# Optimization experiments

Hardware: AMD Instinct MI355X
Metric: run time of the kernel (lower is better)

The kernel has to match this reference:

```python
import jax, jax.numpy as jnp
import numpy as np

B, T, D_IN = 1024, 512, 32   # batch, sequence_length, input_dim
H = 512                      # hidden_dim
P = 96                       # prediction_length
D_OUT = 1                    # output_dim


def setup_inputs() -> dict:
    key = jax.random.key(0)
    ks = jax.random.split(key, 24)
    s = 1.0 / np.sqrt(H)  # PyTorch GRU default init scale
    u = lambda k, shape: jax.random.uniform(k, shape, jnp.float32, -s, s)
    inp = {"x": jax.random.normal(ks[0], (B, T, D_IN), jnp.float32)}
    # Encoder GRU: layer0 input D_IN, layer1 input H. Gate order: r, z, n.
    inp["enc_Wih0"] = u(ks[1], (3 * H, D_IN)); inp["enc_Whh0"] = u(ks[2], (3 * H, H))
    inp["enc_bih0"] = u(ks[3], (3 * H,));      inp["enc_bhh0"] = u(ks[4], (3 * H,))
    inp["enc_Wih1"] = u(ks[5], (3 * H, H));    inp["enc_Whh1"] = u(ks[6], (3 * H, H))
    inp["enc_bih1"] = u(ks[7], (3 * H,));      inp["enc_bhh1"] = u(ks[8], (3 * H,))
    # Decoder GRU: layer0 input D_OUT, layer1 input H.
    inp["dec_Wih0"] = u(ks[9], (3 * H, D_OUT)); inp["dec_Whh0"] = u(ks[10], (3 * H, H))
    inp["dec_bih0"] = u(ks[11], (3 * H,));      inp["dec_bhh0"] = u(ks[12], (3 * H,))
    inp["dec_Wih1"] = u(ks[13], (3 * H, H));    inp["dec_Whh1"] = u(ks[14], (3 * H, H))
    inp["dec_bih1"] = u(ks[15], (3 * H,));      inp["dec_bhh1"] = u(ks[16], (3 * H,))
    # Output projection + learned decoder start token.
    inp["out_W"] = u(ks[17], (D_OUT, H)); inp["out_b"] = u(ks[18], (D_OUT,))
    inp["dec_start"] = jnp.zeros((1, 1, D_OUT), jnp.float32)
    return inp


def gru_cell(x, h, Wih, Whh, bih, bhh):
    # PyTorch GRU cell: r,z,n gate order.
    gi = x @ Wih.T + bih          # [B, 3H]
    gh = h @ Whh.T + bhh          # [B, 3H]
    ir, iz, inn = jnp.split(gi, 3, axis=-1)
    hr, hz, hn = jnp.split(gh, 3, axis=-1)
    r = jax.nn.sigmoid(ir + hr)
    z = jax.nn.sigmoid(iz + hz)
    n = jnp.tanh(inn + r * hn)
    return (1.0 - z) * n + z * h


def reference(x,
              enc_Wih0, enc_Whh0, enc_bih0, enc_bhh0,
              enc_Wih1, enc_Whh1, enc_bih1, enc_bhh1,
              dec_Wih0, dec_Whh0, dec_bih0, dec_bhh0,
              dec_Wih1, dec_Whh1, dec_bih1, dec_bhh1,
              out_W, out_b, dec_start):
    Bsz = x.shape[0]
    h0 = jnp.zeros((Bsz, H), x.dtype)

    def enc_step(carry, xt):
        h1, h2 = carry
        h1 = gru_cell(xt, h1, enc_Wih0, enc_Whh0, enc_bih0, enc_bhh0)
        h2 = gru_cell(h1, h2, enc_Wih1, enc_Whh1, enc_bih1, enc_bhh1)
        return (h1, h2), None

    (h1, h2), _ = jax.lax.scan(enc_step, (h0, h0), jnp.swapaxes(x, 0, 1))

    y0 = jnp.broadcast_to(dec_start[0], (Bsz, D_OUT)).astype(x.dtype)

    def dec_step(carry, _):
        d1, d2, y = carry
        d1 = gru_cell(y, d1, dec_Wih0, dec_Whh0, dec_bih0, dec_bhh0)
        d2 = gru_cell(d1, d2, dec_Wih1, dec_Whh1, dec_bih1, dec_bhh1)
        y = d2 @ out_W.T + out_b  # [B, D_OUT]
        return (d1, d2, y), y

    _, ys = jax.lax.scan(dec_step, (h1, h2, y0), None, length=P)
    return jnp.swapaxes(ys, 0, 1)  # [B, P, D_OUT]
```

## Files before the change

kernel.cpp:

```cpp
#include <hip/hip_runtime.h>

#define HD 512
#define BB 1024
#define TT 512
#define PP 96
#define DIN 32
#define KC_H 16
#define NBLK 256
#define GRPB 16

typedef unsigned short u16;
typedef __attribute__((ext_vector_type(8))) short bf16x8;
typedef __attribute__((ext_vector_type(4))) float f32x4;
typedef __attribute__((address_space(3))) unsigned int lds_u32;
typedef __attribute__((address_space(3))) u16 lds_u16;
typedef __attribute__((address_space(1))) unsigned int glb_u32;

#define WAIT_VM(N) asm volatile("s_waitcnt vmcnt(" #N ")" ::: "memory")
__device__ __forceinline__ void bar_raw() { asm volatile("s_barrier" ::: "memory"); }

template <int N> __device__ __forceinline__ void wvm() {
  if constexpr (N == 0) WAIT_VM(0);
  else if constexpr (N == 5) WAIT_VM(5);
  else if constexpr (N == 10) WAIT_VM(10);
  else if constexpr (N == 13) WAIT_VM(13);
  else if constexpr (N == 20) WAIT_VM(20);
  else if constexpr (N == 26) WAIT_VM(26);
}

__device__ __forceinline__ float bf2f(u16 s) {
  return __uint_as_float(((unsigned)s) << 16);
}
__device__ __forceinline__ u16 f2bf_rne(float f) {
  unsigned u = __float_as_uint(f);
  u += 0x7FFF + ((u >> 16) & 1);
  return (u16)(u >> 16);
}
__device__ __forceinline__ float sigm(float v) { return 1.f / (1.f + __expf(-v)); }
__device__ __forceinline__ float tanh_(float a) {
  return 1.f - 2.f / (__expf(2.f * a) + 1.f);
}

__device__ __forceinline__ bf16x8 load_sc16(const u16* p) {
  bf16x8 r;
  asm volatile("global_load_dwordx4 %0, %1, off sc0 sc1" : "=&v"(r) : "v"(p) : "memory");
  return r;
}
__device__ __forceinline__ void store_sc_u16(u16* p, unsigned v) {
  asm volatile("global_store_short %0, %1, off sc0 sc1" :: "v"(p), "v"(v) : "memory");
}
__device__ __forceinline__ void store_sc_f32(float* p, float v) {
  asm volatile("global_store_dword %0, %1, off sc0 sc1" :: "v"(p), "v"(v) : "memory");
}
__device__ __forceinline__ float load_sc_f32w(const float* p) {
  float v;
  asm volatile("global_load_dword %0, %1, off sc0 sc1\ns_waitcnt vmcnt(0)"
               : "=&v"(v) : "v"(p) : "memory");
  return v;
}
__device__ __forceinline__ unsigned load_sc_u32w(const unsigned* p) {
  unsigned v;
  asm volatile("global_load_dword %0, %1, off sc0 sc1\ns_waitcnt vmcnt(0)"
               : "=&v"(v) : "v"(p) : "memory");
  return v;
}
__device__ __forceinline__ void store_h_sc(u16* H, u16* L, size_t idx, float hv) {
  u16 hi = (u16)(__float_as_uint(hv) >> 16);
  u16 lo = f2bf_rne(hv - bf2f(hi));
  store_sc_u16(H + idx, (unsigned)hi);
  store_sc_u16(L + idx, (unsigned)lo);
}

__global__ void pack_w_kernel(const float* __restrict__ W, int K,
                              u16* __restrict__ out) {
  int tid = blockIdx.x * 256 + threadIdx.x;
  int KC = K >> 5;
  int total = 16 * KC * 2 * 6 * 64;
  if (tid >= total) return;
  int lane = tid & 63;
  int rest = tid >> 6;
  int gs = rest % 6; rest /= 6;
  int fc = rest & 1; rest >>= 1;
  int kc = rest % KC;
  int jb = rest / KC;
  int g = gs >> 1, s = gs & 1;
  int j = jb * 32 + fc * 16 + (lane & 15);
  int k = kc * 32 + (lane >> 4) * 8;
  const float* src = W + (size_t)(g * HD + j) * K + k;
  bf16x8 v;
#pragma unroll
  for (int i = 0; i < 8; ++i) {
    float f = src[i];
    u16 hi = f2bf_rne(f);
    v[i] = (short)((s == 0) ? hi : f2bf_rne(f - bf2f(hi)));
  }
  *(bf16x8*)(out + (size_t)tid * 8) = v;
}

template <int NA> struct AFN { bf16x8 h[NA]; bf16x8 l[NA]; };
template <int NA>
__device__ __forceinline__ void fence_afn(AFN<NA>& a) {
#pragma unroll
  for (int n = 0; n < NA; ++n)
    asm volatile("" : "+v"(a.h[n]), "+v"(a.l[n]));
}

__device__ __forceinline__ void mfma_kc9(const lds_u16* base, int lane,
                                         bf16x8 ah, bf16x8 al,
                                         f32x4& R, f32x4& Z, f32x4& N) {
  typedef __attribute__((address_space(3))) const bf16x8 lds_bf16x8;
  const lds_u16* p = base + lane * 8;
#pragma unroll
  for (int g = 0; g < 3; ++g) {
    f32x4* a = (g == 0) ? &R : (g == 1) ? &Z : &N;
    bf16x8 whi = *(lds_bf16x8*)(p + (g * 2 + 0) * 512);
    bf16x8 wlo = *(lds_bf16x8*)(p + (g * 2 + 1) * 512);
    *a = __builtin_amdgcn_mfma_f32_16x16x32_bf16(ah, whi, *a, 0, 0, 0);
    *a = __builtin_amdgcn_mfma_f32_16x16x32_bf16(al, whi, *a, 0, 0, 0);
    *a = __builtin_amdgcn_mfma_f32_16x16x32_bf16(ah, wlo, *a, 0, 0, 0);
  }
}
__device__ __forceinline__ void mfma_kc9_g(const u16* base, int lane,
                                           bf16x8 ah, bf16x8 al,
                                           f32x4& R, f32x4& Z, f32x4& N) {
  const u16* p = base + lane * 8;
#pragma unroll
  for (int g = 0; g < 3; ++g) {
    f32x4* a = (g == 0) ? &R : (g == 1) ? &Z : &N;
    bf16x8 whi = *(const bf16x8*)(p + (g * 2 + 0) * 512);
    bf16x8 wlo = *(const bf16x8*)(p + (g * 2 + 1) * 512);
    *a = __builtin_amdgcn_mfma_f32_16x16x32_bf16(ah, whi, *a, 0, 0, 0);
    *a = __builtin_amdgcn_mfma_f32_16x16x32_bf16(al, whi, *a, 0, 0, 0);
    *a = __builtin_amdgcn_mfma_f32_16x16x32_bf16(ah, wlo, *a, 0, 0, 0);
  }
}

template <int NS, int NA, int DEPTH>
__device__ __forceinline__ void pipeN(
    u16* ringb,
    const u16* (&Ahi)[NA], const u16* (&Alo)[NA],
    const u16* (&Wjb)[NS], const int (&ai)[NS],
    f32x4* (&acc)[NS][3],
    int row0w, int lane, int wave) {
  constexpr int B = NS * 3 + 2 * NA;
  constexpr int SLOT = NS * 6144;
  const int quad = lane >> 4, n16 = lane & 15;
  const u16* aH[NA]; const u16* aL[NA];
#pragma unroll
  for (int n = 0; n < NA; ++n) {
    aH[n] = Ahi[n] + (size_t)(row0w + n16) * HD + quad * 8;
    aL[n] = Alo[n] + (size_t)(row0w + n16) * HD + quad * 8;
  }
  const u16* srcB[NS * 3]; int dstO[NS * 3];
#pragma unroll
  for (int i = 0; i < NS * 3; ++i) {
    const int p = wave * (NS * 3) + i;
    const int s = p / 12, r = p % 12, f2 = r / 6, j = r % 6;
    const int co = f2 * 3072 + j * 512;
    srcB[i] = Wjb[s] + co + lane * 8;
    dstO[i] = s * 6144 + co;
  }
  u16* pb[DEPTH];
#pragma unroll
  for (int d = 0; d < DEPTH; ++d) pb[d] = ringb + d * SLOT;
  AFN<NA> af[DEPTH];

  auto issueB = [&](int ikc, int si) {
#pragma unroll
    for (int i = 0; i < NS * 3; ++i)
      __builtin_amdgcn_global_load_lds(
          (const glb_u32*)(srcB[i] + (size_t)ikc * 6144),
          (lds_u32*)(pb[si] + dstO[i]), 16, 0, 0);
#pragma unroll
    for (int n = 0; n < NA; ++n) {
      af[si].h[n] = load_sc16(aH[n] + ikc * 32);
      af[si].l[n] = load_sc16(aL[n] + ikc * 32);
    }
  };
  auto cons = [&](int si) {
    fence_afn(af[si]);
#pragma unroll
    for (int s = 0; s < NS; ++s)
#pragma unroll
      for (int f = 0; f < 2; ++f)
        mfma_kc9((const lds_u16*)(pb[si] + s * 6144 + f * 3072), lane,
                 af[si].h[ai[s]], af[si].l[ai[s]],
                 acc[s][0][f], acc[s][1][f], acc[s][2][f]);
  };

  WAIT_VM(0);
#pragma unroll
  for (int p = 0; p < DEPTH - 1; ++p) issueB(p, p);
  if constexpr (DEPTH == 4) {
#pragma unroll 1
    for (int kc = 0; kc < 12; kc += 4) {
      wvm<2 * B>(); bar_raw(); issueB(kc + 3, 3); cons(0);
      wvm<2 * B>(); bar_raw(); issueB(kc + 4, 0); cons(1);
      wvm<2 * B>(); bar_raw(); issueB(kc + 5, 1); cons(2);
      wvm<2 * B>(); bar_raw(); issueB(kc + 6, 2); cons(3);
    }
    wvm<2 * B>(); bar_raw(); issueB(15, 3); cons(0);
    wvm<2 * B>(); bar_raw(); cons(1);
    wvm<B>();     bar_raw(); cons(2);
    wvm<0>();     bar_raw(); cons(3);
  } else {
#pragma unroll 1
    for (int kc = 0; kc < 12; kc += 3) {
      wvm<B>(); bar_raw(); issueB(kc + 2, 2); cons(0);
      wvm<B>(); bar_raw(); issueB(kc + 3, 0); cons(1);
      wvm<B>(); bar_raw(); issueB(kc + 4, 1); cons(2);
    }
    wvm<B>(); bar_raw(); issueB(14, 2); cons(0);
    wvm<B>(); bar_raw(); issueB(15, 0); cons(1);
    wvm<B>(); bar_raw(); cons(2);
    wvm<0>(); bar_raw(); cons(0);
  }
}

__device__ __forceinline__ void x_phase(const float* x, int t, const u16* Wp,
                                        int jb, int row0w, int lane,
                                        f32x4* aR, f32x4* aZ, f32x4* aN) {
  const int quad = lane >> 4, n16 = lane & 15;
  const float* xp = x + (size_t)(row0w + n16) * (TT * DIN) +
                    (size_t)t * DIN + quad * 8;
  f32x4 v0 = *(const f32x4*)xp;
  f32x4 v1 = *(const f32x4*)(xp + 4);
  bf16x8 hi, lo;
#pragma unroll
  for (int i = 0; i < 8; ++i) {
    float f = (i < 4) ? v0[i] : v1[i - 4];
    u16 h = (u16)(__float_as_uint(f) >> 16);
    hi[i] = (short)h;
    lo[i] = (short)f2bf_rne(f - bf2f(h));
  }
#pragma unroll
  for (int f = 0; f < 2; ++f)
    mfma_kc9_g(Wp + ((size_t)jb * 2 + f) * 3072, lane, hi, lo,
               aR[f], aZ[f], aN[f]);
}

__device__ __forceinline__ void gbar(unsigned* gen, unsigned target) {
  WAIT_VM(0);
  __syncthreads();
  if (threadIdx.x == 0) {
    atomicAdd(gen, 1u);
    while (load_sc_u32w(gen) < target) __builtin_amdgcn_s_sleep(2);
  }
  __syncthreads();
}

__device__ __forceinline__ void gru_epi_reg(
    const float* bi, const float* bh, float (*ht)[4],
    u16* hnH, u16* hnL, int col0, int row0w, int quad,
    const f32x4* aR, const f32x4* aZ, const f32x4* aNX, const f32x4* aNH) {
#pragma unroll
  for (int f = 0; f < 2; ++f) {
    const int col = col0 + f * 16;
    const float bir = bi[col],          bhr = bh[col];
    const float biz = bi[HD + col],     bhz = bh[HD + col];
    const float bin = bi[2 * HD + col], bhn = bh[2 * HD + col];
#pragma unroll
    for (int r = 0; r < 4; ++r) {
      const int row = row0w + quad * 4 + r;
      const size_t idx = (size_t)row * HD + col;
      float rr = sigm(aR[f][r] + bir + bhr);
      float zz = sigm(aZ[f][r] + biz + bhz);
      float nn = tanh_(aNX[f][r] + bin + rr * (aNH[f][r] + bhn));
      float hv = (1.f - zz) * nn + zz * ht[f][r];
      ht[f][r] = hv;
      store_h_sc(hnH, hnL, idx, hv);
    }
  }
}

__global__ __launch_bounds__(256, 1)
void gru_persistent_kernel(
    const float* x,
    const u16* pkX0, const u16* pkH0, const float* bi0, const float* bh0,
    const u16* pkX1, const u16* pkH1, const float* bi1, const float* bh1,
    const u16* pkD0H, const float* dbi0, const float* dbh0, const float* dW0,
    const u16* pkD1I, const u16* pkD1H, const float* dbi1, const float* dbh1,
    const float* outW, const float* outb, const float* dstart,
    u16* h1aH, u16* h1aL, u16* h1bH, u16* h1bL,
    u16* h2aH, u16* h2aL, u16* h2bH, u16* h2bL,
    float* yfull, float* dout, unsigned* gen) {
  __shared__ u16 ring[3 * 3 * 6144];
  const int b = blockIdx.x;
  const int jb = (b & 7) * 2 + ((b >> 3) & 1);
  const int row0 = (b >> 4) * 64;
  const int tid = threadIdx.x, wave = tid >> 6, lane = tid & 63;
  const int quad = lane >> 4, n16 = lane & 15;
  const int row0w = row0 + wave * 16;
  const int col0 = jb * 32 + n16;
  u16* ringb = &ring[0];
  const f32x4 z4 = {0.f, 0.f, 0.f, 0.f};
  const size_t jbs = (size_t)jb * (KC_H * 2 * 3072);
  const u16* pkH0j = pkH0 + jbs;
  const u16* pkX1j = pkX1 + jbs;
  const u16* pkH1j = pkH1 + jbs;
  const u16* pkD0Hj = pkD0H + jbs;
  const u16* pkD1Ij = pkD1I + jbs;
  const u16* pkD1Hj = pkD1H + jbs;
  unsigned* geng = gen + ((b >> 4) << 6);

  u16 *h1cH = h1aH, *h1cL = h1aL, *h1nH = h1bH, *h1nL = h1bL;
  u16 *h2cH = h2aH, *h2cL = h2aL, *h2nH = h2bH, *h2nL = h2bL;
  float ht1[2][4] = {{0, 0, 0, 0}, {0, 0, 0, 0}};
  float ht2[2][4] = {{0, 0, 0, 0}, {0, 0, 0, 0}};
  unsigned it = 0;

  for (int k = 0; k <= TT; ++k) {
    f32x4 R0[2] = {z4, z4}, Z0[2] = {z4, z4}, NX0[2] = {z4, z4}, NH0[2] = {z4, z4};
    f32x4 R1[2] = {z4, z4}, Z1[2] = {z4, z4}, NX1[2] = {z4, z4}, NH1[2] = {z4, z4};
    if (k > 0 && k < TT) {
      const u16* Ah[2] = {h1cH, h2cH};
      const u16* Al[2] = {h1cL, h2cL};
      const u16* Wv[3] = {pkH0j, pkX1j, pkH1j};
      const int ai3[3] = {0, 0, 1};
      f32x4* ac[3][3] = {{R0, Z0, NH0}, {R1, Z1, NX1}, {R1, Z1, NH1}};
      pipeN<3, 2, 3>(ringb, Ah, Al, Wv, ai3, ac, row0w, lane, wave);
    } else if (k == 0) {
      const u16* Ah[1] = {h1cH};
      const u16* Al[1] = {h1cL};
      const u16* Wv[1] = {pkH0j};
      const int ai1[1] = {0};
      f32x4* ac[1][3] = {{R0, Z0, NH0}};
      pipeN<1, 1, 4>(ringb, Ah, Al, Wv, ai1, ac, row0w, lane, wave);
    } else {
      const u16* Ah[2] = {h1cH, h2cH};
      const u16* Al[2] = {h1cL, h2cL};
      const u16* Wv[2] = {pkX1j, pkH1j};
      const int ai2[2] = {0, 1};
      f32x4* ac[2][3] = {{R1, Z1, NX1}, {R1, Z1, NH1}};
      pipeN<2, 2, 4>(ringb, Ah, Al, Wv, ai2, ac, row0w, lane, wave);
    }
    if (k < TT) {
      x_phase(x, k, pkX0, jb, row0w, lane, R0, Z0, NX0);
      gru_epi_reg(bi0, bh0, ht1, h1nH, h1nL, col0, row0w, quad, R0, Z0, NX0, NH0);
    }
    if (k > 0) {
      gru_epi_reg(bi1, bh1, ht2, h2nH, h2nL, col0, row0w, quad, R1, Z1, NX1, NH1);
    }
    gbar(geng, GRPB * (++it));
    if (k < TT) { u16* t0 = h1cH; h1cH = h1nH; h1nH = t0;
                  u16* t1 = h1cL; h1cL = h1nL; h1nL = t1; }
    if (k > 0)  { u16* t0 = h2cH; h2cH = h2nH; h2nH = t0;
                  u16* t1 = h2cL; h2cL = h2nL; h2nL = t1; }
  }

  for (int t = 0; t < PP; ++t) {
    {
      f32x4 R[2] = {z4, z4}, Z[2] = {z4, z4}, NH[2] = {z4, z4};
      {
        const u16* Ah[1] = {h1cH};
        const u16* Al[1] = {h1cL};
        const u16* Wv[1] = {pkD0Hj};
        const int ai1[1] = {0};
        f32x4* ac[1][3] = {{R, Z, NH}};
        pipeN<1, 1, 4>(ringb, Ah, Al, Wv, ai1, ac, row0w, lane, wave);
      }
      float yl[4] = {0, 0, 0, 0};
      if (t > 0) {
        const float* yb = yfull + ((t - 1) & 1) * BB;
#pragma unroll
        for (int r = 0; r < 4; ++r) {
          const float* p = yb + (row0w + quad * 4 + r);
          asm volatile("global_load_dword %0, %1, off sc0 sc1"
                       : "=&v"(yl[r]) : "v"(p) : "memory");
        }
        WAIT_VM(0);
#pragma unroll
        for (int r = 0; r < 4; ++r)
          asm volatile("" : "+v"(yl[r]));
      }
      const float ds0 = dstart[0], ob0 = outb[0];
#pragma unroll
      for (int f = 0; f < 2; ++f) {
        const int col = col0 + f * 16;
        const float bir = dbi0[col],          bhr = dbh0[col];
        const float biz = dbi0[HD + col],     bhz = dbh0[HD + col];
        const float bin = dbi0[2 * HD + col], bhn = dbh0[2 * HD + col];
        const float w0r = dW0[col], w0z = dW0[HD + col], w0n = dW0[2 * HD + col];
#pragma unroll
        for (int r = 0; r < 4; ++r) {
          const int row = row0w + quad * 4 + r;
          const size_t idx = (size_t)row * HD + col;
          float yv = (t == 0) ? ds0 : (ob0 + yl[r]);
          if (f == 0 && t > 0 && jb == 0 && n16 == 0)
            dout[(size_t)row * PP + (t - 1)] = yv;
          float rr = sigm(R[f][r] + bir + bhr + yv * w0r);
          float zz = sigm(Z[f][r] + biz + bhz + yv * w0z);
          float nn = tanh_(bin + yv * w0n + rr * (NH[f][r] + bhn));
          float hv = (1.f - zz) * nn + zz * ht1[f][r];
          ht1[f][r] = hv;
          store_h_sc(h1nH, h1nL, idx, hv);
        }
      }
    }
    gbar(geng, GRPB * (++it));
    {
      f32x4 R[2] = {z4, z4}, Z[2] = {z4, z4}, NX[2] = {z4, z4}, NH[2] = {z4, z4};
      {
        const u16* Ah[2] = {h1nH, h2cH};
        const u16* Al[2] = {h1nL, h2cL};
        const u16* Wv[2] = {pkD1Ij, pkD1Hj};
        const int ai2[2] = {0, 1};
        f32x4* ac[2][3] = {{R, Z, NX}, {R, Z, NH}};
        pipeN<2, 2, 4>(ringb, Ah, Al, Wv, ai2, ac, row0w, lane, wave);
      }
      float vs[4] = {0, 0, 0, 0};
#pragma unroll
      for (int f = 0; f < 2; ++f) {
        const int col = col0 + f * 16;
        const float bir = dbi1[col],          bhr = dbh1[col];
        const float biz = dbi1[HD + col],     bhz = dbh1[HD + col];
        const float bin = dbi1[2 * HD + col], bhn = dbh1[2 * HD + col];
        const float wo = outW[col];
#pragma unroll
        for (int r = 0; r < 4; ++r) {
          const int row = row0w + quad * 4 + r;
          const size_t idx = (size_t)row * HD + col;
          float rr = sigm(R[f][r] + bir + bhr);
          float zz = sigm(Z[f][r] + biz + bhz);
          float nn = tanh_(NX[f][r] + bin + rr * (NH[f][r] + bhn));
          float hv = (1.f - zz) * nn + zz * ht2[f][r];
          ht2[f][r] = hv;
          store_h_sc(h2nH, h2nL, idx, hv);
          float v = hv * wo;
#pragma unroll
          for (int off = 1; off < 16; off <<= 1) v += __shfl_xor(v, off, 16);
          vs[r] += v;
        }
      }
      float* yw = yfull + (t & 1) * BB;
      float* yz = yfull + ((t - 1) & 1) * BB;
#pragma unroll
      for (int r = 0; r < 4; ++r) {
        const int row = row0w + quad * 4 + r;
        if (n16 == 0) {
          atomicAdd(yw + row, vs[r]);
          if (t > 0 && jb == 0) store_sc_f32(yz + row, 0.f);
        }
      }
    }
    gbar(geng, GRPB * (++it));
    { u16* t0 = h1cH; h1cH = h1nH; h1nH = t0;
      u16* t1 = h1cL; h1cL = h1nL; h1nL = t1; }
    { u16* t0 = h2cH; h2cH = h2nH; h2nH = t0;
      u16* t1 = h2cL; h2cL = h2nL; h2nL = t1; }
  }

  if ((b & 15) == 0 && tid < 64) {
    int row = row0 + tid;
    float v = load_sc_f32w(yfull + ((PP - 1) & 1) * BB + row);
    dout[(size_t)row * PP + (PP - 1)] = outb[0] + v;
  }
}

extern "C" void kernel_launch(void* const* d_in, const int* in_sizes, int n_in,
                              void* d_out, int out_size, void* d_ws, size_t ws_size,
                              hipStream_t stream) {
  const float* x      = (const float*)d_in[0];
  const float* eW_ih0 = (const float*)d_in[1];
  const float* eW_hh0 = (const float*)d_in[2];
  const float* eb_ih0 = (const float*)d_in[3];
  const float* eb_hh0 = (const float*)d_in[4];
  const float* eW_ih1 = (const float*)d_in[5];
  const float* eW_hh1 = (const float*)d_in[6];
  const float* eb_ih1 = (const float*)d_in[7];
  const float* eb_hh1 = (const float*)d_in[8];
  const float* dW_ih0 = (const float*)d_in[9];
  const float* dW_hh0 = (const float*)d_in[10];
  const float* db_ih0 = (const float*)d_in[11];
  const float* db_hh0 = (const float*)d_in[12];
  const float* dW_ih1 = (const float*)d_in[13];
  const float* dW_hh1 = (const float*)d_in[14];
  const float* db_ih1 = (const float*)d_in[15];
  const float* db_hh1 = (const float*)d_in[16];
  const float* outW   = (const float*)d_in[17];
  const float* outb   = (const float*)d_in[18];
  const float* dstart = (const float*)d_in[19];
  float* out = (float*)d_out;

  char* w = (char*)d_ws;
  size_t off = 0;
  auto carve = [&](size_t bytes) -> void* {
    void* p = w + off;
    off = (off + bytes + 255) & ~(size_t)255;
    return p;
  };
  u16* h1aH = (u16*)carve((size_t)BB * HD * 2); u16* h1aL = (u16*)carve((size_t)BB * HD * 2);
  u16* h1bH = (u16*)carve((size_t)BB * HD * 2); u16* h1bL = (u16*)carve((size_t)BB * HD * 2);
  u16* h2aH = (u16*)carve((size_t)BB * HD * 2); u16* h2aL = (u16*)carve((size_t)BB * HD * 2);
  u16* h2bH = (u16*)carve((size_t)BB * HD * 2); u16* h2bL = (u16*)carve((size_t)BB * HD * 2);
  float* yfull = (float*)carve((size_t)2 * BB * 4);
  unsigned* gen = (unsigned*)carve(4096);
  auto carve_pack = [&](int K) -> u16* {
    return (u16*)carve((size_t)3 * HD * K * 2 * 2);
  };
  u16* pk_e0ih = carve_pack(DIN);
  u16* pk_e0hh = carve_pack(HD);
  u16* pk_e1ih = carve_pack(HD);
  u16* pk_e1hh = carve_pack(HD);
  u16* pk_d0hh = carve_pack(HD);
  u16* pk_d1ih = carve_pack(HD);
  u16* pk_d1hh = carve_pack(HD);

  hipMemsetAsync(h1aH, 0, (size_t)BB * HD * 2, stream);
  hipMemsetAsync(h1aL, 0, (size_t)BB * HD * 2, stream);
  hipMemsetAsync(h2aH, 0, (size_t)BB * HD * 2, stream);
  hipMemsetAsync(h2aL, 0, (size_t)BB * HD * 2, stream);
  hipMemsetAsync(yfull, 0, (size_t)2 * BB * 4, stream);
  hipMemsetAsync(gen, 0, 4096, stream);

  auto pack = [&](const float* W, int K, u16* dst) {
    int total = 16 * (K >> 5) * 2 * 6 * 64;
    pack_w_kernel<<<(total + 255) / 256, 256, 0, stream>>>(W, K, dst);
  };
  pack(eW_ih0, DIN, pk_e0ih);
  pack(eW_hh0, HD, pk_e0hh);
  pack(eW_ih1, HD, pk_e1ih);
  pack(eW_hh1, HD, pk_e1hh);
  pack(dW_hh0, HD, pk_d0hh);
  pack(dW_ih1, HD, pk_d1ih);
  pack(dW_hh1, HD, pk_d1hh);

  gru_persistent_kernel<<<NBLK, 256, 0, stream>>>(
      x, pk_e0ih, pk_e0hh, eb_ih0, eb_hh0,
      pk_e1ih, pk_e1hh, eb_ih1, eb_hh1,
      pk_d0hh, db_ih0, db_hh0, dW_ih0,
      pk_d1ih, pk_d1hh, db_ih1, db_hh1,
      outW, outb, dstart,
      h1aH, h1aL, h1bH, h1bL, h2aH, h2aL, h2bH, h2bL,
      yfull, out, gen);
}
```

Measured before the change: 16.27 ms.

## Split grid barrier and prefetch next step's weights and x-projection during the wait

Splits the global barrier into arrive and wait halves. Between them it issues the first two k-chunks of the next phase's weight tiles into the LDS ring and computes the next timestep's input (x) projection. The pipeline therefore starts with weights already in flight, and the barrier wait latency is hidden behind useful work. The fixed 3-deep ring replaces the 3/4-depth variants, which changes the vmcnt wait counts and adds register pressure for the carried x accumulators.

```diff
diff --git a/kernel.cpp b/kernel.cpp
--- a/kernel.cpp
+++ b/kernel.cpp
@@ -21,11 +21,11 @@
 
 template <int N> __device__ __forceinline__ void wvm() {
   if constexpr (N == 0) WAIT_VM(0);
+  else if constexpr (N == 2) WAIT_VM(2);
+  else if constexpr (N == 4) WAIT_VM(4);
   else if constexpr (N == 5) WAIT_VM(5);
   else if constexpr (N == 10) WAIT_VM(10);
   else if constexpr (N == 13) WAIT_VM(13);
-  else if constexpr (N == 20) WAIT_VM(20);
-  else if constexpr (N == 26) WAIT_VM(26);
 }
 
 __device__ __forceinline__ float bf2f(u16 s) {
@@ -135,23 +135,11 @@
   }
 }
 
-template <int NS, int NA, int DEPTH>
-__device__ __forceinline__ void pipeN(
-    u16* ringb,
-    const u16* (&Ahi)[NA], const u16* (&Alo)[NA],
-    const u16* (&Wjb)[NS], const int (&ai)[NS],
-    f32x4* (&acc)[NS][3],
-    int row0w, int lane, int wave) {
-  constexpr int B = NS * 3 + 2 * NA;
-  constexpr int SLOT = NS * 6144;
-  const int quad = lane >> 4, n16 = lane & 15;
-  const u16* aH[NA]; const u16* aL[NA];
-#pragma unroll
-  for (int n = 0; n < NA; ++n) {
-    aH[n] = Ahi[n] + (size_t)(row0w + n16) * HD + quad * 8;
-    aL[n] = Alo[n] + (size_t)(row0w + n16) * HD + quad * 8;
-  }
-  const u16* srcB[NS * 3]; int dstO[NS * 3];
+template <int NS>
+__device__ __forceinline__ void piece_map(const u16* const (&Wjb)[NS],
+                                          int lane, int wave,
+                                          const u16* (&srcB)[NS * 3],
+                                          int (&dstO)[NS * 3]) {
 #pragma unroll
   for (int i = 0; i < NS * 3; ++i) {
     const int p = wave * (NS * 3) + i;
@@ -160,66 +148,89 @@
     srcB[i] = Wjb[s] + co + lane * 8;
     dstO[i] = s * 6144 + co;
   }
-  u16* pb[DEPTH];
-#pragma unroll
-  for (int d = 0; d < DEPTH; ++d) pb[d] = ringb + d * SLOT;
-  AFN<NA> af[DEPTH];
-
-  auto issueB = [&](int ikc, int si) {
+}
+
+template <int NS>
+__device__ __forceinline__ void stageW2(u16* ringb, const u16* const (&Wjb)[NS],
+                                        int lane, int wave) {
+  const u16* srcB[NS * 3]; int dstO[NS * 3];
+  piece_map<NS>(Wjb, lane, wave, srcB, dstO);
+#pragma unroll
+  for (int ikc = 0; ikc < 2; ++ikc)
+#pragma unroll
+    for (int i = 0; i < NS * 3; ++i)
+      __builtin_amdgcn_global_load_lds(
+          (const glb_u32*)(srcB[i] + (size_t)ikc * 6144),
+          (lds_u32*)(ringb + (size_t)ikc * NS * 6144 + dstO[i]), 16, 0, 0);
+}
+
+template <int NS, int NA>
+__device__ __forceinline__ void pipePre(
+    u16* ringb,
+    const u16* const (&Ahi)[NA], const u16* const (&Alo)[NA],
+    const u16* const (&Wjb)[NS], const int (&ai)[NS],
+    f32x4* (&acc)[NS][3],
+    int row0w, int lane, int wave) {
+  constexpr int B = NS * 3 + 2 * NA;
+  constexpr int A2 = 2 * NA;
+  constexpr int SLOT = NS * 6144;
+  const int quad = lane >> 4, n16 = lane & 15;
+  const u16* aH[NA]; const u16* aL[NA];
+#pragma unroll
+  for (int n = 0; n < NA; ++n) {
+    aH[n] = Ahi[n] + (size_t)(row0w + n16) * HD + quad * 8;
+    aL[n] = Alo[n] + (size_t)(row0w + n16) * HD + quad * 8;
+  }
+  const u16* srcB[NS * 3]; int dstO[NS * 3];
+  piece_map<NS>(Wjb, lane, wave, srcB, dstO);
+  u16* pb[3] = {ringb, ringb + SLOT, ringb + 2 * SLOT};
+  AFN<NA> af0, af1, af2;
+
+  auto issueA = [&](int ikc, AFN<NA>& dst) {
+#pragma unroll
+    for (int n = 0; n < NA; ++n) {
+      dst.h[n] = load_sc16(aH[n] + ikc * 32);
+      dst.l[n] = load_sc16(aL[n] + ikc * 32);
+    }
+  };
+  auto issueB = [&](int ikc, int si, AFN<NA>& dst) {
 #pragma unroll
     for (int i = 0; i < NS * 3; ++i)
       __builtin_amdgcn_global_load_lds(
           (const glb_u32*)(srcB[i] + (size_t)ikc * 6144),
           (lds_u32*)(pb[si] + dstO[i]), 16, 0, 0);
-#pragma unroll
-    for (int n = 0; n < NA; ++n) {
-      af[si].h[n] = load_sc16(aH[n] + ikc * 32);
-      af[si].l[n] = load_sc16(aL[n] + ikc * 32);
-    }
+    issueA(ikc, dst);
   };
-  auto cons = [&](int si) {
-    fence_afn(af[si]);
+  auto cons = [&](int si, AFN<NA>& a) {
+    fence_afn(a);
 #pragma unroll
     for (int s = 0; s < NS; ++s)
 #pragma unroll
       for (int f = 0; f < 2; ++f)
         mfma_kc9((const lds_u16*)(pb[si] + s * 6144 + f * 3072), lane,
-                 af[si].h[ai[s]], af[si].l[ai[s]],
+                 a.h[ai[s]], a.l[ai[s]],
                  acc[s][0][f], acc[s][1][f], acc[s][2][f]);
   };
 
   WAIT_VM(0);
-#pragma unroll
-  for (int p = 0; p < DEPTH - 1; ++p) issueB(p, p);
-  if constexpr (DEPTH == 4) {
+  issueA(0, af0);
+  issueA(1, af1);
+  wvm<A2>(); bar_raw(); issueB(2, 2, af2); cons(0, af0);
+  wvm<B>();  bar_raw(); issueB(3, 0, af0); cons(1, af1);
 #pragma unroll 1
-    for (int kc = 0; kc < 12; kc += 4) {
-      wvm<2 * B>(); bar_raw(); issueB(kc + 3, 3); cons(0);
-      wvm<2 * B>(); bar_raw(); issueB(kc + 4, 0); cons(1);
-      wvm<2 * B>(); bar_raw(); issueB(kc + 5, 1); cons(2);
-      wvm<2 * B>(); bar_raw(); issueB(kc + 6, 2); cons(3);
-    }
-    wvm<2 * B>(); bar_raw(); issueB(15, 3); cons(0);
-    wvm<2 * B>(); bar_raw(); cons(1);
-    wvm<B>();     bar_raw(); cons(2);
-    wvm<0>();     bar_raw(); cons(3);
-  } else {
-#pragma unroll 1
-    for (int kc = 0; kc < 12; kc += 3) {
-      wvm<B>(); bar_raw(); issueB(kc + 2, 2); cons(0);
-      wvm<B>(); bar_raw(); issueB(kc + 3, 0); cons(1);
-      wvm<B>(); bar_raw(); issueB(kc + 4, 1); cons(2);
-    }
-    wvm<B>(); bar_raw(); issueB(14, 2); cons(0);
-    wvm<B>(); bar_raw(); issueB(15, 0); cons(1);
-    wvm<B>(); bar_raw(); cons(2);
-    wvm<0>(); bar_raw(); cons(0);
-  }
-}
-
-__device__ __forceinline__ void x_phase(const float* x, int t, const u16* Wp,
-                                        int jb, int row0w, int lane,
-                                        f32x4* aR, f32x4* aZ, f32x4* aN) {
+  for (int q = 0; q < 4; ++q) {
+    const int base = 4 + q * 3;
+    wvm<B>(); bar_raw(); issueB(base + 0, 1, af1); cons(2, af2);
+    wvm<B>(); bar_raw(); issueB(base + 1, 2, af2); cons(0, af0);
+    wvm<B>(); bar_raw(); issueB(base + 2, 0, af0); cons(1, af1);
+  }
+  wvm<B>(); bar_raw(); cons(2, af2);
+  wvm<0>(); bar_raw(); cons(0, af0);
+}
+
+__device__ __forceinline__ void x_acc(const float* x, int t, const u16* Wp,
+                                      int jb, int row0w, int lane,
+                                      f32x4* aR, f32x4* aZ, f32x4* aN) {
   const int quad = lane >> 4, n16 = lane & 15;
   const float* xp = x + (size_t)(row0w + n16) * (TT * DIN) +
                     (size_t)t * DIN + quad * 8;
@@ -239,11 +250,13 @@
                aR[f], aZ[f], aN[f]);
 }
 
-__device__ __forceinline__ void gbar(unsigned* gen, unsigned target) {
+__device__ __forceinline__ void gbar_arrive(unsigned* gen) {
   WAIT_VM(0);
   __syncthreads();
+  if (threadIdx.x == 0) atomicAdd(gen, 1u);
+}
+__device__ __forceinline__ void gbar_wait(unsigned* gen, unsigned target) {
   if (threadIdx.x == 0) {
-    atomicAdd(gen, 1u);
     while (load_sc_u32w(gen) < target) __builtin_amdgcn_s_sleep(2);
   }
   __syncthreads();
@@ -309,39 +322,66 @@
   float ht2[2][4] = {{0, 0, 0, 0}, {0, 0, 0, 0}};
   unsigned it = 0;
 
+  f32x4 xR[2] = {z4, z4}, xZ[2] = {z4, z4}, xN[2] = {z4, z4};
+  {
+    const u16* Wv1[1] = {pkH0j};
+    stageW2<1>(ringb, Wv1, lane, wave);
+    x_acc(x, 0, pkX0, jb, row0w, lane, xR, xZ, xN);
+  }
+
   for (int k = 0; k <= TT; ++k) {
-    f32x4 R0[2] = {z4, z4}, Z0[2] = {z4, z4}, NX0[2] = {z4, z4}, NH0[2] = {z4, z4};
+    f32x4 R0[2], Z0[2], NX0[2], NH0[2] = {z4, z4};
     f32x4 R1[2] = {z4, z4}, Z1[2] = {z4, z4}, NX1[2] = {z4, z4}, NH1[2] = {z4, z4};
+    if (k < TT) {
+      R0[0] = xR[0]; R0[1] = xR[1];
+      Z0[0] = xZ[0]; Z0[1] = xZ[1];
+      NX0[0] = xN[0]; NX0[1] = xN[1];
+    } else {
+      R0[0] = z4; R0[1] = z4; Z0[0] = z4; Z0[1] = z4; NX0[0] = z4; NX0[1] = z4;
+    }
     if (k > 0 && k < TT) {
       const u16* Ah[2] = {h1cH, h2cH};
       const u16* Al[2] = {h1cL, h2cL};
       const u16* Wv[3] = {pkH0j, pkX1j, pkH1j};
       const int ai3[3] = {0, 0, 1};
       f32x4* ac[3][3] = {{R0, Z0, NH0}, {R1, Z1, NX1}, {R1, Z1, NH1}};
-      pipeN<3, 2, 3>(ringb, Ah, Al, Wv, ai3, ac, row0w, lane, wave);
+      pipePre<3, 2>(ringb, Ah, Al, Wv, ai3, ac, row0w, lane, wave);
     } else if (k == 0) {
       const u16* Ah[1] = {h1cH};
       const u16* Al[1] = {h1cL};
       const u16* Wv[1] = {pkH0j};
       const int ai1[1] = {0};
       f32x4* ac[1][3] = {{R0, Z0, NH0}};
-      pipeN<1, 1, 4>(ringb, Ah, Al, Wv, ai1, ac, row0w, lane, wave);
+      pipePre<1, 1>(ringb, Ah, Al, Wv, ai1, ac, row0w, lane, wave);
     } else {
       const u16* Ah[2] = {h1cH, h2cH};
       const u16* Al[2] = {h1cL, h2cL};
       const u16* Wv[2] = {pkX1j, pkH1j};
       const int ai2[2] = {0, 1};
       f32x4* ac[2][3] = {{R1, Z1, NX1}, {R1, Z1, NH1}};
-      pipeN<2, 2, 4>(ringb, Ah, Al, Wv, ai2, ac, row0w, lane, wave);
-    }
-    if (k < TT) {
-      x_phase(x, k, pkX0, jb, row0w, lane, R0, Z0, NX0);
+      pipePre<2, 2>(ringb, Ah, Al, Wv, ai2, ac, row0w, lane, wave);
+    }
+    if (k < TT)
       gru_epi_reg(bi0, bh0, ht1, h1nH, h1nL, col0, row0w, quad, R0, Z0, NX0, NH0);
-    }
-    if (k > 0) {
+    if (k > 0)
       gru_epi_reg(bi1, bh1, ht2, h2nH, h2nL, col0, row0w, quad, R1, Z1, NX1, NH1);
-    }
-    gbar(geng, GRPB * (++it));
+    ++it;
+    gbar_arrive(geng);
+    if (k + 1 < TT) {
+      xR[0] = z4; xR[1] = z4; xZ[0] = z4; xZ[1] = z4; xN[0] = z4; xN[1] = z4;
+      x_acc(x, k + 1, pkX0, jb, row0w, lane, xR, xZ, xN);
+    }
+    if (k + 1 < TT) {
+      const u16* Wv3[3] = {pkH0j, pkX1j, pkH1j};
+      stageW2<3>(ringb, Wv3, lane, wave);
+    } else if (k + 1 == TT) {
+      const u16* Wv2[2] = {pkX1j, pkH1j};
+      stageW2<2>(ringb, Wv2, lane, wave);
+    } else {
+      const u16* Wv1[1] = {pkD0Hj};
+      stageW2<1>(ringb, Wv1, lane, wave);
+    }
+    gbar_wait(geng, GRPB * it);
     if (k < TT) { u16* t0 = h1cH; h1cH = h1nH; h1nH = t0;
                   u16* t1 = h1cL; h1cL = h1nL; h1nL = t1; }
     if (k > 0)  { u16* t0 = h2cH; h2cH = h2nH; h2nH = t0;
@@ -357,7 +397,7 @@
         const u16* Wv[1] = {pkD0Hj};
         const int ai1[1] = {0};
         f32x4* ac[1][3] = {{R, Z, NH}};
-        pipeN<1, 1, 4>(ringb, Ah, Al, Wv, ai1, ac, row0w, lane, wave);
+        pipePre<1, 1>(ringb, Ah, Al, Wv, ai1, ac, row0w, lane, wave);
       }
       float yl[4] = {0, 0, 0, 0};
       if (t > 0) {
@@ -397,7 +437,13 @@
         }
       }
     }
-    gbar(geng, GRPB * (++it));
+    ++it;
+    gbar_arrive(geng);
+    {
+      const u16* Wv2[2] = {pkD1Ij, pkD1Hj};
+      stageW2<2>(ringb, Wv2, lane, wave);
+    }
+    gbar_wait(geng, GRPB * it);
     {
       f32x4 R[2] = {z4, z4}, Z[2] = {z4, z4}, NX[2] = {z4, z4}, NH[2] = {z4, z4};
       {
@@ -406,7 +452,7 @@
         const u16* Wv[2] = {pkD1Ij, pkD1Hj};
         const int ai2[2] = {0, 1};
         f32x4* ac[2][3] = {{R, Z, NX}, {R, Z, NH}};
-        pipeN<2, 2, 4>(ringb, Ah, Al, Wv, ai2, ac, row0w, lane, wave);
+        pipePre<2, 2>(ringb, Ah, Al, Wv, ai2, ac, row0w, lane, wave);
       }
       float vs[4] = {0, 0, 0, 0};
 #pragma unroll
@@ -443,7 +489,13 @@
         }
       }
     }
-    gbar(geng, GRPB * (++it));
+    ++it;
+    gbar_arrive(geng);
+    if (t + 1 < PP) {
+      const u16* Wv1[1] = {pkD0Hj};
+      stageW2<1>(ringb, Wv1, lane, wave);
+    }
+    gbar_wait(geng, GRPB * it);
     { u16* t0 = h1cH; h1cH = h1nH; h1nH = t0;
       u16* t1 = h1cL; h1cL = h1nL; h1nL = t1; }
     { u16* t0 = h2cH; h2cH = h2nH; h2nH = t0;
```

New measurement: 16.13 ms. About the same (-0.8%).
